# Kernel tuning notes

Hardware: AMD Instinct MI355X
Metric: run time of the kernel (lower is better)

## Reference

```python
import math
import jax, jax.numpy as jnp
import numpy as np
from jax.scipy.special import erf

D = 128                # cubic box / image size (even)
B, T = 4, 2            # particles, candidate poses per particle
GRID_DIST_DEGS = 8.0
GRID_STEP_DEGS = 2.0
PIXEL_SIZE = 1.5       # Angstrom / px
MAX_SHIFT_FRACTION = 0.2
TOP_K = 2
HALF_PARTICLE = 0.5 * D


def _rot_z(a):
    c, s = jnp.cos(a), jnp.sin(a)
    z, o = jnp.zeros_like(a), jnp.ones_like(a)
    return jnp.stack([jnp.stack([c, -s, z], -1),
                      jnp.stack([s, c, z], -1),
                      jnp.stack([z, z, o], -1)], -2)


def _rot_y(a):
    c, s = jnp.cos(a), jnp.sin(a)
    z, o = jnp.zeros_like(a), jnp.ones_like(a)
    return jnp.stack([jnp.stack([c, z, s], -1),
                      jnp.stack([z, o, z], -1),
                      jnp.stack([-s, z, c], -1)], -2)


def _euler_zyz_to_matrix(ang):
    # RELION convention ZYZ: R = Rz(a) @ Ry(b) @ Rz(c)
    return _rot_z(ang[..., 0]) @ _rot_y(ang[..., 1]) @ _rot_z(ang[..., 2])


def _so3_grid_rotmats():
    n = math.ceil(GRID_DIST_DEGS / GRID_STEP_DEGS)
    n = n if n % 2 == 1 else n + 1
    half = GRID_DIST_DEGS / 2.0
    a = np.linspace(-half, half, n)
    g = np.stack(np.meshgrid(a, a, a, indexing='ij'), -1).reshape(-1, 3)
    return _euler_zyz_to_matrix(jnp.deg2rad(jnp.asarray(g, jnp.float32)))


def _compute_dft(vol):
    # sinc^2 gridding pre-filter, then fftshifted rfftn of fftshifted volume
    d = vol.shape[-1]
    f = jnp.fft.fftshift(jnp.fft.fftfreq(d)).astype(vol.dtype)
    fz, fy, fx = jnp.meshgrid(f, f, f, indexing='ij')
    r = jnp.sqrt(fz * fz + fy * fy + fx * fx)
    vol = vol * jnp.sinc(r) ** 2
    dft = jnp.fft.rfftn(jnp.fft.fftshift(vol, axes=(-3, -2, -1)), axes=(-3, -2, -1))
    return jnp.fft.fftshift(dft, axes=(-3, -2))


def _trilinear_complex(vol, z, y, x):
    # trilinear interpolation into a complex 3D array, zero outside bounds
    Dz, Dy, Dx = vol.shape
    z0f, y0f, x0f = jnp.floor(z), jnp.floor(y), jnp.floor(x)
    fz, fy, fx = z - z0f, y - y0f, x - x0f
    z0, y0, x0 = z0f.astype(jnp.int32), y0f.astype(jnp.int32), x0f.astype(jnp.int32)

    def corner(zi, yi, xi, w):
        valid = (zi >= 0) & (zi < Dz) & (yi >= 0) & (yi < Dy) & (xi >= 0) & (xi < Dx)
        v = vol[jnp.clip(zi, 0, Dz - 1), jnp.clip(yi, 0, Dy - 1), jnp.clip(xi, 0, Dx - 1)]
        return jnp.where(valid, v * w, jnp.zeros((), vol.dtype))

    out = corner(z0, y0, x0, (1 - fz) * (1 - fy) * (1 - fx))
    out = out + corner(z0, y0, x0 + 1, (1 - fz) * (1 - fy) * fx)
    out = out + corner(z0, y0 + 1, x0, (1 - fz) * fy * (1 - fx))
    out = out + corner(z0, y0 + 1, x0 + 1, (1 - fz) * fy * fx)
    out = out + corner(z0 + 1, y0, x0, fz * (1 - fy) * (1 - fx))
    out = out + corner(z0 + 1, y0, x0 + 1, fz * (1 - fy) * fx)
    out = out + corner(z0 + 1, y0 + 1, x0, fz * fy * (1 - fx))
    out = out + corner(z0 + 1, y0 + 1, x0 + 1, fz * fy * fx)
    return out


def _extract_central_slices_rfft_3d(vol_rfft, d, rotmats):
    # rotated central-slice extraction from a fftshifted rfft 3D volume
    fy = jnp.fft.fftshift(jnp.fft.fftfreq(d)).astype(jnp.float32)
    fx = jnp.fft.rfftfreq(d).astype(jnp.float32)
    gy, gx = jnp.meshgrid(fy, fx, indexing='ij')            # (H, Wr)
    coords = jnp.stack([jnp.zeros_like(gy), gy, gx], -1)    # zyx, z=0 plane
    Rzyx = rotmats[..., ::-1, ::-1]                         # xyz rotmat -> zyx
    rot = jnp.einsum('...ij,hwj->...hwi', Rzyx, coords)     # (...,H,Wr,3)
    conj_mask = rot[..., 2] < 0                             # redundant half
    rot = jnp.where(conj_mask[..., None], -rot, rot)
    zi = rot[..., 0] * d + d // 2
    yi = rot[..., 1] * d + d // 2
    xi = rot[..., 2] * d
    s = _trilinear_complex(vol_rfft, zi, yi, xi)
    return jnp.where(conj_mask, jnp.conj(s), s)


def _forward(vol, imgs, ctf, rotmats, grid_rotmats):
    d = vol.shape[-1]
    vol_rfft = _compute_dft(vol)                            # (d, d, d//2+1)
    # _real_to_fourier
    fimg = jnp.fft.fftshift(
        jnp.fft.rfftn(jnp.fft.fftshift(imgs, axes=(-2, -1)), axes=(-2, -1)),
        axes=(-2,))                                         # (B, d, d//2+1)
    # compose pose candidates with the local SO3 grid: rotmats @ grid_rotmats
    exp_R = jnp.einsum('gjk,btij->btgik', grid_rotmats, rotmats)   # (B,T,G,3,3)
    projs = _extract_central_slices_rfft_3d(vol_rfft, d, exp_R)    # (B,T,G,H,Wr)
    projs = projs * ctf[:, None, None]
    # correlate_dft_2d
    prod = fimg[:, None, None] * jnp.conj(projs)
    prod = jnp.fft.ifftshift(prod, axes=(-2,))
    corrs = jnp.fft.ifftshift(jnp.fft.irfftn(prod, s=(d, d), axes=(-2, -1)),
                              axes=(-2, -1))                # (B,T,G,d,d) real
    # constrained peak search within max_shift_fraction window
    delta = math.ceil(d * (1.0 - MAX_SHIFT_FRACTION) / 2)
    h0 = delta
    c = corrs[..., h0:d - delta, h0:d - delta]
    maxJ = jnp.max(c, -1)
    argJ = jnp.argmax(c, -1)
    perImgCorr = jnp.max(maxJ, -1)                          # (B,T,G)
    argI = jnp.argmax(maxJ, -1)
    col = jnp.take_along_axis(argJ, argI[..., None], -1)[..., 0]
    shiftsXY = jnp.stack([h0 + col, h0 + argI], -1)         # (B,T,G,2) as (x,y)
    b = perImgCorr.shape[0]
    nrots = perImgCorr.shape[2]
    flat = perImgCorr.reshape(b, -1)                        # (B, T*G)
    maxCorrs, maxIdxs = jax.lax.top_k(flat, TOP_K)
    bestShifts = jnp.take_along_axis(shiftsXY.reshape(b, -1, 2),
                                     maxIdxs[..., None], axis=1)   # (B,K,2)
    mean = jnp.mean(flat, -1, keepdims=True)
    std = jnp.std(flat, -1, keepdims=True, ddof=1)
    comparedWeight = 0.5 * (1.0 + erf((maxCorrs - mean) / (std * 1.4142135623730951)))
    predShiftsAngs = -(bestShifts.astype(jnp.float32) - HALF_PARTICLE) * PIXEL_SIZE
    predRotMats = grid_rotmats[maxIdxs % nrots]             # (B,K,3,3)
    return maxCorrs, predRotMats, predShiftsAngs, comparedWeight


def setup_inputs() -> dict:
    key = jax.random.key(0)
    kv, ki, kc, kr = jax.random.split(key, 4)
    vol = jax.random.normal(kv, (D, D, D), jnp.float32)
    imgs = jax.random.normal(ki, (B, D, D), jnp.float32)
    ctf = jax.random.uniform(kc, (B, D, D // 2 + 1), jnp.float32, -1.0, 1.0)
    ang = jax.random.uniform(kr, (B, T, 3), jnp.float32, -np.pi, np.pi)
    rotmats = _euler_zyz_to_matrix(ang)
    grid_rotmats = _so3_grid_rotmats()
    return {"vol": vol, "imgs": imgs, "ctf": ctf, "rotmats": rotmats,
            "grid_rotmats": grid_rotmats}


def reference(vol, imgs, ctf, rotmats, grid_rotmats):
    return _forward(vol, imgs, ctf, rotmats, grid_rotmats)
```

## Files before the change

kernel.cpp:

```cpp
#include <hip/hip_runtime.h>
#include <math.h>
#include <float.h>

#define DD   128
#define KX   65
#define NB   4
#define NTT  2
#define NG   125
#define NBTG (NB*NTT*NG)
#define WIN  24
#define H0   52

#define PZ  132
#define PY  132
#define PX  68
#define PROW  PX
#define PPLANE (PY*PX)

typedef float f4 __attribute__((ext_vector_type(4), aligned(8)));

__device__ __forceinline__ float2 cmul(float2 a, float2 b){
    return make_float2(a.x*b.x - a.y*b.y, a.x*b.y + a.y*b.x);
}

__device__ __forceinline__ void make_tw(float2* sTw, int tid){
    if (tid < 128){
        float s, c;
        sincosf((float)tid * (float)(M_PI/64.0), &s, &c);
        sTw[tid] = make_float2(c, s);
    }
}

__global__ __launch_bounds__(256) void k_stageA(const float* __restrict__ vol,
                       const float* __restrict__ imgs,
                       float2* __restrict__ A1, float2* __restrict__ B1){
    __shared__ float2 sZ [16*DD];
    __shared__ float2 sZ2[16*DD];
    __shared__ float2 sTw[128];
    int tid = threadIdx.x;
    int bid = blockIdx.x;
    make_tw(sTw, tid);
    __syncthreads();

    if (bid < 512){
        int z = bid >> 2, q = bid & 3;
        int y0 = q*32;
        float fz = (z-64)*(1.0f/128.0f);
        for (int i = tid; i < 16*DD; i += 256){
            int p = i >> 7, x = i & 127;
            int yA = y0 + 2*p;
            float fx = (x-64)*(1.0f/128.0f);
            float fyA = (yA-64)*(1.0f/128.0f);
            float fyB = fyA + (1.0f/128.0f);
            float b2 = fz*fz + fx*fx;
            float rA = sqrtf(b2 + fyA*fyA);
            float rB = sqrtf(b2 + fyB*fyB);
            float sA = (rA > 0.f) ? (sinf((float)M_PI*rA)/((float)M_PI*rA)) : 1.f;
            float sB = (rB > 0.f) ? (sinf((float)M_PI*rB)/((float)M_PI*rB)) : 1.f;
            float a = vol[(z*DD + yA)*DD + x] * sA * sA;
            float b = vol[(z*DD + yA+1)*DD + x] * sB * sB;
            sZ[i] = make_float2(a, b);
        }
        __syncthreads();
        for (int i = tid; i < 16*32; i += 256){
            int p = i >> 5, x1 = i & 31;
            int b0 = p*DD + x1;
            float2 a = sZ[b0], bb = sZ[b0+32], c2 = sZ[b0+64], d = sZ[b0+96];
            float acx=a.x+c2.x, acy=a.y+c2.y;
            float amx=a.x-c2.x, amy=a.y-c2.y;
            float bdx=bb.x+d.x, bdy=bb.y+d.y;
            float bmx=bb.x-d.x, bmy=bb.y-d.y;
            sZ[b0   ] = make_float2(acx+bdx, acy+bdy);
            sZ[b0+32] = make_float2(amx+bmy, amy-bmx);
            sZ[b0+64] = make_float2(acx-bdx, acy-bdy);
            sZ[b0+96] = make_float2(amx-bmy, amy+bmx);
        }
        __syncthreads();
        for (int i = tid; i < 16*32; i += 256){
            int p = i >> 5, r5 = i & 31;
            int c = r5 >> 3, x2 = r5 & 7;
            int b0 = p*DD + 32*c + x2;
            float2 u0 = sZ[b0], u1 = sZ[b0+8], u2 = sZ[b0+16], u3 = sZ[b0+24];
            float2 w1 = sTw[(8*c)&127];  w1.y = -w1.y;
            float2 w2 = sTw[(16*c)&127]; w2.y = -w2.y;
            float2 w3 = sTw[(24*c)&127]; w3.y = -w3.y;
            float2 t1 = cmul(u1,w1), t2 = cmul(u2,w2), t3 = cmul(u3,w3);
            float2 pp = make_float2(u0.x+t2.x, u0.y+t2.y);
            float2 qq = make_float2(u0.x-t2.x, u0.y-t2.y);
            float2 rr = make_float2(t1.x+t3.x, t1.y+t3.y);
            float2 ss = make_float2(t1.x-t3.x, t1.y-t3.y);
            sZ[b0   ] = make_float2(pp.x+rr.x, pp.y+rr.y);
            sZ[b0+8 ] = make_float2(qq.x+ss.y, qq.y-ss.x);
            sZ[b0+16] = make_float2(pp.x-rr.x, pp.y-rr.y);
            sZ[b0+24] = make_float2(qq.x-ss.y, qq.y+ss.x);
        }
        __syncthreads();
        for (int i = tid; i < 16*DD; i += 256){
            int p = i >> 7, k = i & 127;
            int c = k & 3, s = (k >> 2) & 3;
            const float2* v = &sZ[p*DD + 32*c + 8*s];
            float ar0=0,ai0=0,ar1=0,ai1=0;
            int j = 0;
            #pragma unroll
            for (int x2 = 0; x2 < 8; x2 += 2){
                float2 v0 = v[x2], v1 = v[x2+1];
                float2 e0 = sTw[j]; int jn = (j + k)&127;
                float2 e1 = sTw[jn];
                ar0 += v0.x*e0.x + v0.y*e0.y;  ai0 += v0.y*e0.x - v0.x*e0.y;
                ar1 += v1.x*e1.x + v1.y*e1.y;  ai1 += v1.y*e1.x - v1.x*e1.y;
                j = (jn + k)&127;
            }
            sZ2[i] = make_float2(ar0+ar1, ai0+ai1);
        }
        __syncthreads();
        for (int i = tid; i < 16*KX; i += 256){
            int p = i / KX, k = i - p*KX;
            float2 Zk = sZ2[p*DD + k];
            float2 Zm = sZ2[p*DD + ((128-k)&127)];
            float2 A = make_float2(0.5f*(Zk.x+Zm.x), 0.5f*(Zk.y-Zm.y));
            float Dx = Zk.x - Zm.x, Dy = Zk.y + Zm.y;
            float2 Bv = make_float2(0.5f*Dy, -0.5f*Dx);
            int yA = y0 + 2*p;
            A1[(z*DD + yA  )*KX + k] = A;
            A1[(z*DD + yA+1)*KX + k] = Bv;
        }
    } else {
        int o = (bid - 512)*256 + tid;
        if (o >= NB*DD*KX) return;
        int b = o / (DD*KX);
        int r = o - b*DD*KX;
        int y = r / KX, k = r - y*KX;
        const float* row = imgs + (b*DD + y)*DD;
        float ar0=0,ai0=0,ar1=0,ai1=0,ar2=0,ai2=0,ar3=0,ai3=0;
        int i0=0, i1=k&127, i2=(2*k)&127, i3=(3*k)&127;
        int st = (4*k)&127;
        for (int x = 0; x < DD; x += 4){
            float v0=row[x], v1=row[x+1], v2=row[x+2], v3=row[x+3];
            float2 e0=sTw[i0], e1=sTw[i1], e2=sTw[i2], e3=sTw[i3];
            ar0 += v0*e0.x; ai0 -= v0*e0.y;
            ar1 += v1*e1.x; ai1 -= v1*e1.y;
            ar2 += v2*e2.x; ai2 -= v2*e2.y;
            ar3 += v3*e3.x; ai3 -= v3*e3.y;
            i0=(i0+st)&127; i1=(i1+st)&127; i2=(i2+st)&127; i3=(i3+st)&127;
        }
        B1[o] = make_float2(ar0+ar1+ar2+ar3, ai0+ai1+ai2+ai3);
    }
}

__global__ __launch_bounds__(256) void k_stageB(const float2* __restrict__ A1,
                       const float* __restrict__ ctf, const float2* __restrict__ B1,
                       float2* __restrict__ A2, float2* __restrict__ Fc){
    __shared__ float2 sU[32*KX];
    __shared__ float2 sTw[128];
    int tid = threadIdx.x;
    int bid = blockIdx.x;
    make_tw(sTw, tid);
    __syncthreads();

    if (bid < 512){
        int z = bid >> 2, c = bid & 3;
        const float2* base = A1 + z*DD*KX;
        for (int i = tid; i < 32*KX; i += 256){
            int n = i / KX, kk = i - n*KX;
            float2 a  = base[(n    )*KX + kk];
            float2 bb = base[(n+32)*KX + kk];
            float2 c2 = base[(n+64)*KX + kk];
            float2 d  = base[(n+96)*KX + kk];
            float acx = a.x + c2.x, acy = a.y + c2.y;
            float amx = a.x - c2.x, amy = a.y - c2.y;
            float bdx = bb.x + d.x, bdy = bb.y + d.y;
            float bmx = bb.x - d.x, bmy = bb.y - d.y;
            float2 u;
            if (c == 0)      u = make_float2(acx + bdx, acy + bdy);
            else if (c == 2) u = make_float2(acx - bdx, acy - bdy);
            else if (c == 1) u = make_float2(amx + bmy, amy - bmx);
            else             u = make_float2(amx - bmy, amy + bmx);
            sU[i] = u;
        }
        __syncthreads();
        float2 w1 = sTw[(8*c)&127];  w1.y = -w1.y;
        float2 w2 = sTw[(16*c)&127]; w2.y = -w2.y;
        float2 w3 = sTw[(24*c)&127]; w3.y = -w3.y;
        for (int i = tid; i < 8*KX; i += 256){
            int n2 = i / KX, kk = i - n2*KX;
            int b0 = n2*KX + kk;
            float2 u0 = sU[b0], u1 = sU[b0+8*KX], u2 = sU[b0+16*KX], u3 = sU[b0+24*KX];
            float2 t1 = cmul(u1,w1), t2 = cmul(u2,w2), t3 = cmul(u3,w3);
            float2 p = make_float2(u0.x+t2.x, u0.y+t2.y);
            float2 q = make_float2(u0.x-t2.x, u0.y-t2.y);
            float2 r = make_float2(t1.x+t3.x, t1.y+t3.y);
            float2 s = make_float2(t1.x-t3.x, t1.y-t3.y);
            sU[b0       ] = make_float2(p.x+r.x, p.y+r.y);
            sU[b0+ 8*KX ] = make_float2(q.x+s.y, q.y-s.x);
            sU[b0+16*KX ] = make_float2(p.x-r.x, p.y-r.y);
            sU[b0+24*KX ] = make_float2(q.x-s.y, q.y+s.x);
        }
        __syncthreads();
        for (int o = tid; o < 32*KX; o += 256){
            int m = o / KX, kk = o - m*KX;
            int ky = 4*m + c;
            int s4 = m & 3;
            const float2* v = &sU[(8*s4)*KX + kk];
            float ar0=0,ai0=0,ar1=0,ai1=0;
            int j = 0;
            #pragma unroll
            for (int n2 = 0; n2 < 8; n2 += 2){
                float2 v0 = v[n2*KX], v1 = v[(n2+1)*KX];
                float2 e0 = sTw[j]; int jn = (j + ky)&127;
                float2 e1 = sTw[jn];
                ar0 += v0.x*e0.x + v0.y*e0.y;  ai0 += v0.y*e0.x - v0.x*e0.y;
                ar1 += v1.x*e1.x + v1.y*e1.y;  ai1 += v1.y*e1.x - v1.x*e1.y;
                j = (jn + ky)&127;
            }
            A2[(z*DD + ky)*KX + kk] = make_float2(ar0+ar1, ai0+ai1);
        }
    } else {
        int o = (bid - 512)*256 + tid;
        if (o >= NB*DD*KX) return;
        int b = o / (DD*KX);
        int r = o - b*DD*KX;
        int h = r / KX, k = r - h*KX;
        int kky = (h + 64) & 127;
        const float2* col = B1 + b*DD*KX + k;
        float ar0=0,ai0=0,ar1=0,ai1=0,ar2=0,ai2=0,ar3=0,ai3=0;
        int i0=0, i1=kky&127, i2=(2*kky)&127, i3=(3*kky)&127;
        int st = (4*kky)&127;
        for (int y = 0; y < DD; y += 4){
            float2 v0=col[(y+0)*KX], v1=col[(y+1)*KX];
            float2 v2=col[(y+2)*KX], v3=col[(y+3)*KX];
            float2 e0=sTw[i0], e1=sTw[i1], e2=sTw[i2], e3=sTw[i3];
            ar0 += v0.x*e0.x + v0.y*e0.y;  ai0 += v0.y*e0.x - v0.x*e0.y;
            ar1 += v1.x*e1.x + v1.y*e1.y;  ai1 += v1.y*e1.x - v1.x*e1.y;
            ar2 += v2.x*e2.x + v2.y*e2.y;  ai2 += v2.y*e2.x - v2.x*e2.y;
            ar3 += v3.x*e3.x + v3.y*e3.y;  ai3 += v3.y*e3.x - v3.x*e3.y;
            i0=(i0+st)&127; i1=(i1+st)&127; i2=(i2+st)&127; i3=(i3+st)&127;
        }
        float sgn = ((h + k)&1) ? -1.f : 1.f;
        float cf = ctf[o];
        Fc[o] = make_float2((ar0+ar1+ar2+ar3)*sgn*cf, (ai0+ai1+ai2+ai3)*sgn*cf);
    }
}

__global__ __launch_bounds__(256) void k_volD(const float2* __restrict__ A2,
                       float2* __restrict__ VrP){
    __shared__ float2 sU[32*KX];
    __shared__ float2 sTw[128];
    int tid = threadIdx.x;
    int bid = blockIdx.x;
    int ky = bid >> 2, c = bid & 3;
    make_tw(sTw, tid);
    __syncthreads();
    const float2* base = A2 + ky*KX;
    for (int i = tid; i < 32*KX; i += 256){
        int n = i / KX, kk = i - n*KX;
        float2 a  = base[(n    )*DD*KX + kk];
        float2 bb = base[(n+32)*DD*KX + kk];
        float2 c2 = base[(n+64)*DD*KX + kk];
        float2 d  = base[(n+96)*DD*KX + kk];
        float acx = a.x + c2.x, acy = a.y + c2.y;
        float amx = a.x - c2.x, amy = a.y - c2.y;
        float bdx = bb.x + d.x, bdy = bb.y + d.y;
        float bmx = bb.x - d.x, bmy = bb.y - d.y;
        float2 u;
        if (c == 0)      u = make_float2(acx + bdx, acy + bdy);
        else if (c == 2) u = make_float2(acx - bdx, acy - bdy);
        else if (c == 1) u = make_float2(amx + bmy, amy - bmx);
        else             u = make_float2(amx - bmy, amy + bmx);
        sU[i] = u;
    }
    __syncthreads();
    float2 w1 = sTw[(8*c)&127];  w1.y = -w1.y;
    float2 w2 = sTw[(16*c)&127]; w2.y = -w2.y;
    float2 w3 = sTw[(24*c)&127]; w3.y = -w3.y;
    for (int i = tid; i < 8*KX; i += 256){
        int n2 = i / KX, kk = i - n2*KX;
        int b0 = n2*KX + kk;
        float2 u0 = sU[b0], u1 = sU[b0+8*KX], u2 = sU[b0+16*KX], u3 = sU[b0+24*KX];
        float2 t1 = cmul(u1,w1), t2 = cmul(u2,w2), t3 = cmul(u3,w3);
        float2 p = make_float2(u0.x+t2.x, u0.y+t2.y);
        float2 q = make_float2(u0.x-t2.x, u0.y-t2.y);
        float2 r = make_float2(t1.x+t3.x, t1.y+t3.y);
        float2 s = make_float2(t1.x-t3.x, t1.y-t3.y);
        sU[b0       ] = make_float2(p.x+r.x, p.y+r.y);
        sU[b0+ 8*KX ] = make_float2(q.x+s.y, q.y-s.x);
        sU[b0+16*KX ] = make_float2(p.x-r.x, p.y-r.y);
        sU[b0+24*KX ] = make_float2(q.x-s.y, q.y+s.x);
    }
    __syncthreads();
    int hy = (ky + 64) & 127;
    for (int o = tid; o < 32*KX; o += 256){
        int m = o / KX, kk = o - m*KX;
        int kz = 4*m + c;
        int hz = (kz + 64) & 127;
        int s4 = m & 3;
        const float2* v = &sU[(8*s4)*KX + kk];
        float ar0=0,ai0=0,ar1=0,ai1=0;
        int j = 0;
        #pragma unroll
        for (int n2 = 0; n2 < 8; n2 += 2){
            float2 v0 = v[n2*KX], v1 = v[(n2+1)*KX];
            float2 e0 = sTw[j]; int jn = (j + kz)&127;
            float2 e1 = sTw[jn];
            ar0 += v0.x*e0.x + v0.y*e0.y;  ai0 += v0.y*e0.x - v0.x*e0.y;
            ar1 += v1.x*e1.x + v1.y*e1.y;  ai1 += v1.y*e1.x - v1.x*e1.y;
            j = (jn + kz)&127;
        }
        float sgn = ((hz + hy + kk) & 1) ? -1.f : 1.f;
        VrP[((hz+1)*PY + (hy+1))*PX + kk] = make_float2((ar0+ar1)*sgn, (ai0+ai1)*sgn);
    }
}

__global__ __launch_bounds__(256,4) void k_main(
    const float2* __restrict__ VrP, const float2* __restrict__ Fc,
    const float* __restrict__ rotm, const float* __restrict__ grid,
    float* __restrict__ resVal, int2* __restrict__ resShift)
{
    __shared__ float2 sP[DD*17];
    __shared__ float2 sT[WIN*KX];
    __shared__ float2 sTw[128];
    __shared__ float  sM[9];
    __shared__ float  swv[4];
    __shared__ int    swi[4];

    int tid = threadIdx.x;
    int blk = blockIdx.x;
    int b  = blk / (NTT*NG);
    int rr = blk - b*NTT*NG;
    int t  = rr / NG;
    int g  = rr - t*NG;

    make_tw(sTw, tid);
    if (tid < 9){
        int i = tid/3, k = tid - 3*i;
        const float* R  = rotm + (b*NTT + t)*9;
        const float* Gm = grid + g*9;
        sM[tid] = R[i*3+0]*Gm[0*3+k] + R[i*3+1]*Gm[1*3+k] + R[i*3+2]*Gm[2*3+k];
    }
    __syncthreads();

    float M00=sM[0], M01=sM[1], M10=sM[3], M11=sM[4], M20=sM[6], M21=sM[7];
    const float2* FcB = Fc + b*DD*KX;

    const int KB[4]  = {0,17,34,51};
    const int NKc[4] = {17,17,17,14};
    #pragma unroll
    for (int cc = 0; cc < 4; ++cc){
        const int kbase = KB[cc];
        const int Nk    = NKc[cc];

        #pragma unroll 2
        for (int idx = tid; idx < DD*Nk; idx += 256){
            int h = idx / Nk, kk = idx - h*Nk;
            int w = kbase + kk;
            float hf = (float)(h - 64);
            float wf = (float)w;
            float xi = M01*hf + M00*wf;
            float zi = M21*hf + M20*wf + 64.f;
            float yi = M11*hf + M10*wf + 64.f;
            bool neg = xi < 0.f;
            if (neg){ xi = -xi; zi = 128.f - zi; yi = 128.f - yi; }
            xi = fminf(xi, 65.f);
            zi = fminf(fmaxf(zi, -1.f), 129.f);
            yi = fminf(fmaxf(yi, -1.f), 129.f);
            float z0f = floorf(zi), y0f = floorf(yi), x0f = floorf(xi);
            float fz2 = zi - z0f, fy2 = yi - y0f, fx2 = xi - x0f;
            int z0 = (int)z0f, y0 = (int)y0f, x0 = (int)x0f;
            int basei = ((z0+1)*PY + (y0+1))*PX + x0;
            f4 v00 = *reinterpret_cast<const f4*>(VrP + basei);
            f4 v01 = *reinterpret_cast<const f4*>(VrP + basei + PROW);
            f4 v10 = *reinterpret_cast<const f4*>(VrP + basei + PPLANE);
            f4 v11 = *reinterpret_cast<const f4*>(VrP + basei + PPLANE + PROW);
            float2 f = FcB[h*KX + w];
            float gx = 1.f - fx2;
            float r00 = v00.x*gx + v00.z*fx2, i00 = v00.y*gx + v00.w*fx2;
            float r01 = v01.x*gx + v01.z*fx2, i01 = v01.y*gx + v01.w*fx2;
            float r10 = v10.x*gx + v10.z*fx2, i10 = v10.y*gx + v10.w*fx2;
            float r11 = v11.x*gx + v11.z*fx2, i11 = v11.y*gx + v11.w*fx2;
            float gz = 1.f - fz2, gy = 1.f - fy2;
            float w00 = gz*gy, w01 = gz*fy2, w10 = fz2*gy, w11 = fz2*fy2;
            float sr = r00*w00 + r01*w01 + r10*w10 + r11*w11;
            float si = i00*w00 + i01*w01 + i10*w10 + i11*w11;
            if (neg) si = -si;
            sP[h*17 + kk] = make_float2(f.x*sr + f.y*si, f.y*sr - f.x*si);
        }
        __syncthreads();

        for (int i = tid; i < 32*Nk; i += 256){
            int n = i / Nk, kk = i - n*Nk;
            int o0 = n*17 + kk;
            float2 a  = sP[o0];
            float2 bb = sP[o0 + 32*17];
            float2 c2 = sP[o0 + 64*17];
            float2 d  = sP[o0 + 96*17];
            float acx = a.x + c2.x, acy = a.y + c2.y;
            float amx = a.x - c2.x, amy = a.y - c2.y;
            float bdx = bb.x + d.x, bdy = bb.y + d.y;
            float bmx = bb.x - d.x, bmy = bb.y - d.y;
            sP[o0        ] = make_float2(acx + bdx, acy + bdy);
            sP[o0 + 32*17] = make_float2(amx - bmy, amy + bmx);
            sP[o0 + 64*17] = make_float2(acx - bdx, acy - bdy);
            sP[o0 + 96*17] = make_float2(amx + bmy, amy - bmx);
        }
        __syncthreads();

        for (int i = tid; i < 32*Nk; i += 256){
            int q = i / Nk, kk = i - q*Nk;
            int c = q >> 3, n2 = q & 7;
            int b0 = (32*c + n2)*17 + kk;
            float2 u0 = sP[b0], u1 = sP[b0+8*17], u2 = sP[b0+16*17], u3 = sP[b0+24*17];
            float2 w1 = sTw[(8*c)&127], w2 = sTw[(16*c)&127], w3 = sTw[(24*c)&127];
            float2 t1 = cmul(u1,w1), t2 = cmul(u2,w2), t3 = cmul(u3,w3);
            float2 p  = make_float2(u0.x+t2.x, u0.y+t2.y);
            float2 qq = make_float2(u0.x-t2.x, u0.y-t2.y);
            float2 r  = make_float2(t1.x+t3.x, t1.y+t3.y);
            float2 s  = make_float2(t1.x-t3.x, t1.y-t3.y);
            sP[b0       ] = make_float2(p.x+r.x,  p.y+r.y);
            sP[b0+ 8*17 ] = make_float2(qq.x-s.y, qq.y+s.x);
            sP[b0+16*17 ] = make_float2(p.x-r.x,  p.y-r.y);
            sP[b0+24*17 ] = make_float2(qq.x+s.y, qq.y-s.x);
        }
        __syncthreads();

        for (int o = tid; o < WIN*Nk; o += 256){
            int a = o / Nk, kk = o - a*Nk;
            int ry = (116 + a) & 127;
            int c = ry & 3, s4 = (ry >> 2) & 3;
            const float2* v = &sP[(32*c + 8*s4)*17 + kk];
            float ar0=0,ai0=0,ar1=0,ai1=0;
            int j = 0;
            #pragma unroll
            for (int n2 = 0; n2 < 8; n2 += 2){
                float2 v0 = v[n2*17], v1 = v[(n2+1)*17];
                float2 e0 = sTw[j]; int jn = (j + ry)&127;
                float2 e1 = sTw[jn];
                ar0 += v0.x*e0.x - v0.y*e0.y;  ai0 += v0.x*e0.y + v0.y*e0.x;
                ar1 += v1.x*e1.x - v1.y*e1.y;  ai1 += v1.x*e1.y + v1.y*e1.x;
                j = (jn + ry)&127;
            }
            float sgn = (a & 1) ? -(1.f/128.f) : (1.f/128.f);
            sT[a*KX + kbase + kk] = make_float2((ar0+ar1)*sgn, (ai0+ai1)*sgn);
        }
        __syncthreads();
    }

    float2* sPf = sP;
    for (int o = tid; o < WIN*31; o += 256){
        int a = o / 31, km1 = o - a*31;
        int k = km1 + 1;
        const float2* Trow = &sT[a*KX];
        float2 T1 = Trow[k], T2 = Trow[64-k];
        sPf[a*31 + km1]       = make_float2(T1.x + T2.x, T1.y - T2.y);
        sPf[744 + a*31 + km1] = make_float2(T1.x - T2.x, T1.y + T2.y);
    }
    __syncthreads();

    float* sC = reinterpret_cast<float*>(sP + 1488);
    for (int o = tid; o < WIN*WIN; o += 256){
        int a = o / WIN, bx = o - a*WIN;
        int rx = (116 + bx) & 127;
        const float2* Trow = &sT[a*KX];
        float2 T32 = Trow[32];
        float base = Trow[0].x + ((bx & 1) ? -Trow[64].x : Trow[64].x);
        int r4 = rx & 3;
        base += (r4==0) ?  2.f*T32.x : (r4==1) ? -2.f*T32.y
              : (r4==2) ? -2.f*T32.x :  2.f*T32.y;
        const float2* A = sPf + ((bx & 1) ? 744 : 0) + a*31 - 1;
        float acc0=0.f, acc1=0.f;
        int j1 = rx, j2 = (2*rx)&127;
        int st = (2*rx)&127;
        for (int k = 1; k < 31; k += 2){
            float2 e1 = sTw[j1]; float2 A1v = A[k];
            float2 e2 = sTw[j2]; float2 A2v = A[k+1];
            acc0 += A1v.x*e1.x - A1v.y*e1.y;
            acc1 += A2v.x*e2.x - A2v.y*e2.y;
            j1=(j1+st)&127; j2=(j2+st)&127;
        }
        {
            float2 e = sTw[(31*rx)&127]; float2 Av = A[31];
            acc0 += Av.x*e.x - Av.y*e.y;
        }
        sC[o] = (base + 2.f*(acc0+acc1))*(1.f/128.f);
    }
    __syncthreads();

    float best = -FLT_MAX; int bidx = 0x7fffffff;
    for (int i = tid; i < WIN*WIN; i += 256){
        float v = sC[i];
        if (v > best){ best = v; bidx = i; }
    }
    #pragma unroll
    for (int s = 32; s > 0; s >>= 1){
        float ov = __shfl_xor(best, s, 64);
        int   oi = __shfl_xor(bidx, s, 64);
        if (ov > best || (ov == best && oi < bidx)){ best = ov; bidx = oi; }
    }
    if ((tid & 63) == 0){ swv[tid>>6] = best; swi[tid>>6] = bidx; }
    __syncthreads();
    if (tid == 0){
        float bv = swv[0]; int bi = swi[0];
        #pragma unroll
        for (int w2 = 1; w2 < 4; ++w2){
            if (swv[w2] > bv || (swv[w2] == bv && swi[w2] < bi)){ bv = swv[w2]; bi = swi[w2]; }
        }
        int a = bi / WIN, bx = bi - a*WIN;
        resVal[blk] = bv;
        resShift[blk] = make_int2(H0 + bx, H0 + a);
    }
}

__global__ __launch_bounds__(256) void k_final(const float* __restrict__ resVal,
                        const int2* __restrict__ resShift,
                        const float* __restrict__ grid, float* __restrict__ out)
{
    __shared__ float sv[256];
    __shared__ int   si[256];
    __shared__ float sr[256];
    __shared__ float sMean;
    const int N = NTT*NG;
    int b = blockIdx.x, tid = threadIdx.x;
    const float* v = resVal + b*N;
    float myv = (tid < N) ? v[tid] : -FLT_MAX;

    sv[tid] = myv; si[tid] = (tid < N) ? tid : 0x7fffffff;
    __syncthreads();
    for (int s = 128; s > 0; s >>= 1){
        if (tid < s){
            float v2 = sv[tid+s]; int i2 = si[tid+s];
            if (v2 > sv[tid] || (v2 == sv[tid] && i2 < si[tid])){ sv[tid]=v2; si[tid]=i2; }
        }
        __syncthreads();
    }
    float v0 = sv[0]; int i0 = si[0];
    __syncthreads();

    bool act = (tid < N) && (tid != i0);
    sv[tid] = act ? myv : -FLT_MAX; si[tid] = act ? tid : 0x7fffffff;
    __syncthreads();
    for (int s = 128; s > 0; s >>= 1){
        if (tid < s){
            float v2 = sv[tid+s]; int i2 = si[tid+s];
            if (v2 > sv[tid] || (v2 == sv[tid] && i2 < si[tid])){ sv[tid]=v2; si[tid]=i2; }
        }
        __syncthreads();
    }
    float v1 = sv[0]; int i1 = si[0];
    __syncthreads();

    sr[tid] = (tid < N) ? myv : 0.f;
    __syncthreads();
    for (int s = 128; s > 0; s >>= 1){
        if (tid < s) sr[tid] += sr[tid+s];
        __syncthreads();
    }
    if (tid == 0) sMean = sr[0] / (float)N;
    __syncthreads();
    float mean = sMean;

    float d = (tid < N) ? (myv - mean) : 0.f;
    sr[tid] = d*d;
    __syncthreads();
    for (int s = 128; s > 0; s >>= 1){
        if (tid < s) sr[tid] += sr[tid+s];
        __syncthreads();
    }

    if (tid == 0){
        float stdv = sqrtf(sr[0] / (float)(N - 1));
        float vals[2] = {v0, v1};
        int   idxs[2] = {i0, i1};
        for (int k = 0; k < 2; ++k){
            out[b*2 + k] = vals[k];
            int gi = idxs[k] % NG;
            for (int j = 0; j < 9; ++j) out[8 + (b*2+k)*9 + j] = grid[gi*9 + j];
            int2 sh = resShift[b*N + idxs[k]];
            out[80 + (b*2+k)*2 + 0] = -((float)sh.x - 64.f)*1.5f;
            out[80 + (b*2+k)*2 + 1] = -((float)sh.y - 64.f)*1.5f;
            out[96 + b*2 + k] = 0.5f*(1.f + erff((vals[k] - mean)/(stdv*1.41421356237309515f)));
        }
    }
}

extern "C" void kernel_launch(void* const* d_in, const int* in_sizes, int n_in,
                              void* d_out, int out_size, void* d_ws, size_t ws_size,
                              hipStream_t stream)
{
    const float* vol  = (const float*)d_in[0];
    const float* imgs = (const float*)d_in[1];
    const float* ctf  = (const float*)d_in[2];
    const float* rotm = (const float*)d_in[3];
    const float* grid = (const float*)d_in[4];
    float* out = (float*)d_out;

    const size_t A1_BYTES  = (size_t)DD*DD*KX*sizeof(float2);
    const size_t B1_BYTES  = (size_t)NB*DD*KX*sizeof(float2);
    const size_t VRP_BYTES = (size_t)PZ*PY*PX*sizeof(float2);

    char* ws = (char*)d_ws;
    float2* A1  = (float2*)(ws);
    float2* B1  = (float2*)(ws + A1_BYTES);
    float2* VrP = (float2*)(ws);
    size_t off = VRP_BYTES;
    float2* A2 = (float2*)(ws + off); off += A1_BYTES;
    float2* Fc = (float2*)(ws + off); off += B1_BYTES;
    float* resVal = (float*)(ws + off); off += (size_t)NBTG*sizeof(float);
    int2* resShift = (int2*)(ws + off); off += (size_t)NBTG*sizeof(int2);

    k_stageA<<<642, 256, 0, stream>>>(vol, imgs, A1, B1);
    k_stageB<<<642, 256, 0, stream>>>(A1, ctf, B1, A2, Fc);
    hipMemsetAsync(VrP, 0, VRP_BYTES, stream);
    k_volD  <<<512, 256, 0, stream>>>(A2, VrP);
    k_main  <<<NBTG,256, 0, stream>>>(VrP, Fc, rotm, grid, resVal, resShift);
    k_final <<<NB,  256, 0, stream>>>(resVal, resShift, grid, out);
}
```

Baseline: 121.1 us.

## Zero only VrP halo in volD, remap main block order, batch gather loads

Drops the full-volume memset of the padded volume and has k_volD zero only the halo cells that the interior writes never touch. k_main's block index is permuted so that consecutive blocks come from different particle/pose combinations, which changes cache locality across workgroups. The gather loop is manually unrolled so each thread issues two points' worth of trilinear loads before doing any arithmetic, exposing more memory-level parallelism. The risks are higher register pressure and correctness depending on the halo index math exactly covering all uncovered cells.

Measured after the change: 119.2 us. Within noise of the previous version (-1.6%).

```diff
diff --git a/kernel.cpp b/kernel.cpp
--- a/kernel.cpp
+++ b/kernel.cpp
@@ -16,6 +16,7 @@
 #define PX  68
 #define PROW  PX
 #define PPLANE (PY*PX)
+#define HALO_N 119872
 
 typedef float f4 __attribute__((ext_vector_type(4), aligned(8)));
 
@@ -249,7 +250,39 @@
     int bid = blockIdx.x;
     int ky = bid >> 2, c = bid & 3;
     make_tw(sTw, tid);
-    __syncthreads();
+
+    {
+        int hidx = bid*234 + tid;
+        hidx = bid*256 + tid;
+        if (hidx < HALO_N){
+            int z, y, x;
+            if (hidx < 35904){
+                int p = hidx / 8976;
+                int r = hidx - p*8976;
+                z = (p == 0) ? 0 : (128 + p);
+                y = r / 68;
+                x = r - 68*y;
+            } else if (hidx < 70720){
+                int h2 = hidx - 35904;
+                int zz = h2 / 272;
+                int r = h2 - zz*272;
+                z = 1 + zz;
+                int p = r / 68;
+                y = (p == 0) ? 0 : (128 + p);
+                x = r - 68*p;
+            } else {
+                int h3 = hidx - 70720;
+                int zz = h3 / 384;
+                int r = h3 - zz*384;
+                z = 1 + zz;
+                y = 1 + r/3;
+                x = 65 + (r - 3*(r/3));
+            }
+            VrP[(z*PY + y)*PX + x] = make_float2(0.f, 0.f);
+        }
+    }
+    __syncthreads();
+
     const float2* base = A2 + ky*KX;
     for (int i = tid; i < 32*KX; i += 256){
         int n = i / KX, kk = i - n*KX;
@@ -323,7 +356,8 @@
     __shared__ int    swi[4];
 
     int tid = threadIdx.x;
-    int blk = blockIdx.x;
+    int nb  = blockIdx.x;
+    int blk = (nb & 7)*125 + (nb >> 3);
     int b  = blk / (NTT*NG);
     int rr = blk - b*NTT*NG;
     int t  = rr / NG;
@@ -347,41 +381,82 @@
     for (int cc = 0; cc < 4; ++cc){
         const int kbase = KB[cc];
         const int Nk    = NKc[cc];
-
-        #pragma unroll 2
-        for (int idx = tid; idx < DD*Nk; idx += 256){
-            int h = idx / Nk, kk = idx - h*Nk;
-            int w = kbase + kk;
-            float hf = (float)(h - 64);
-            float wf = (float)w;
-            float xi = M01*hf + M00*wf;
-            float zi = M21*hf + M20*wf + 64.f;
-            float yi = M11*hf + M10*wf + 64.f;
-            bool neg = xi < 0.f;
-            if (neg){ xi = -xi; zi = 128.f - zi; yi = 128.f - yi; }
-            xi = fminf(xi, 65.f);
-            zi = fminf(fmaxf(zi, -1.f), 129.f);
-            yi = fminf(fmaxf(yi, -1.f), 129.f);
-            float z0f = floorf(zi), y0f = floorf(yi), x0f = floorf(xi);
-            float fz2 = zi - z0f, fy2 = yi - y0f, fx2 = xi - x0f;
-            int z0 = (int)z0f, y0 = (int)y0f, x0 = (int)x0f;
-            int basei = ((z0+1)*PY + (y0+1))*PX + x0;
-            f4 v00 = *reinterpret_cast<const f4*>(VrP + basei);
-            f4 v01 = *reinterpret_cast<const f4*>(VrP + basei + PROW);
-            f4 v10 = *reinterpret_cast<const f4*>(VrP + basei + PPLANE);
-            f4 v11 = *reinterpret_cast<const f4*>(VrP + basei + PPLANE + PROW);
-            float2 f = FcB[h*KX + w];
-            float gx = 1.f - fx2;
-            float r00 = v00.x*gx + v00.z*fx2, i00 = v00.y*gx + v00.w*fx2;
-            float r01 = v01.x*gx + v01.z*fx2, i01 = v01.y*gx + v01.w*fx2;
-            float r10 = v10.x*gx + v10.z*fx2, i10 = v10.y*gx + v10.w*fx2;
-            float r11 = v11.x*gx + v11.z*fx2, i11 = v11.y*gx + v11.w*fx2;
-            float gz = 1.f - fz2, gy = 1.f - fy2;
-            float w00 = gz*gy, w01 = gz*fy2, w10 = fz2*gy, w11 = fz2*fy2;
-            float sr = r00*w00 + r01*w01 + r10*w10 + r11*w11;
-            float si = i00*w00 + i01*w01 + i10*w10 + i11*w11;
-            if (neg) si = -si;
-            sP[h*17 + kk] = make_float2(f.x*sr + f.y*si, f.y*sr - f.x*si);
+        const int total = DD*Nk;
+
+        for (int base = 0; base < total; base += 512){
+            int iA = base + tid;
+            int iB = iA + 256;
+            bool vA = iA < total, vB = iB < total;
+            int cA = vA ? iA : 0, cB = vB ? iB : 0;
+
+            int hA = cA / Nk, kkA = cA - hA*Nk;  int wA = kbase + kkA;
+            int hB = cB / Nk, kkB = cB - hB*Nk;  int wB = kbase + kkB;
+
+            float hfA = (float)(hA - 64), wfA = (float)wA;
+            float xiA = M01*hfA + M00*wfA;
+            float ziA = M21*hfA + M20*wfA + 64.f;
+            float yiA = M11*hfA + M10*wfA + 64.f;
+            bool negA = xiA < 0.f;
+            if (negA){ xiA = -xiA; ziA = 128.f - ziA; yiA = 128.f - yiA; }
+            xiA = fminf(xiA, 65.f);
+            ziA = fminf(fmaxf(ziA, -1.f), 129.f);
+            yiA = fminf(fmaxf(yiA, -1.f), 129.f);
+            float zfA = floorf(ziA), yfA = floorf(yiA), xfA = floorf(xiA);
+            float fzA = ziA - zfA, fyA = yiA - yfA, fxA = xiA - xfA;
+            int z0A = (int)zfA, y0A = (int)yfA, x0A = (int)xfA;
+            int baseiA = ((z0A+1)*PY + (y0A+1))*PX + x0A;
+
+            float hfB = (float)(hB - 64), wfB = (float)wB;
+            float xiB = M01*hfB + M00*wfB;
+            float ziB = M21*hfB + M20*wfB + 64.f;
+            float yiB = M11*hfB + M10*wfB + 64.f;
+            bool negB = xiB < 0.f;
+            if (negB){ xiB = -xiB; ziB = 128.f - ziB; yiB = 128.f - yiB; }
+            xiB = fminf(xiB, 65.f);
+            ziB = fminf(fmaxf(ziB, -1.f), 129.f);
+            yiB = fminf(fmaxf(yiB, -1.f), 129.f);
+            float zfB = floorf(ziB), yfB = floorf(yiB), xfB = floorf(xiB);
+            float fzB = ziB - zfB, fyB = yiB - yfB, fxB = xiB - xfB;
+            int z0B = (int)zfB, y0B = (int)yfB, x0B = (int)xfB;
+            int baseiB = ((z0B+1)*PY + (y0B+1))*PX + x0B;
+
+            f4 a00 = *reinterpret_cast<const f4*>(VrP + baseiA);
+            f4 a01 = *reinterpret_cast<const f4*>(VrP + baseiA + PROW);
+            f4 a10 = *reinterpret_cast<const f4*>(VrP + baseiA + PPLANE);
+            f4 a11 = *reinterpret_cast<const f4*>(VrP + baseiA + PPLANE + PROW);
+            f4 b00 = *reinterpret_cast<const f4*>(VrP + baseiB);
+            f4 b01 = *reinterpret_cast<const f4*>(VrP + baseiB + PROW);
+            f4 b10 = *reinterpret_cast<const f4*>(VrP + baseiB + PPLANE);
+            f4 b11 = *reinterpret_cast<const f4*>(VrP + baseiB + PPLANE + PROW);
+            float2 fA = FcB[hA*KX + wA];
+            float2 fB = FcB[hB*KX + wB];
+
+            {
+                float gx = 1.f - fxA;
+                float r00 = a00.x*gx + a00.z*fxA, i00 = a00.y*gx + a00.w*fxA;
+                float r01 = a01.x*gx + a01.z*fxA, i01 = a01.y*gx + a01.w*fxA;
+                float r10 = a10.x*gx + a10.z*fxA, i10 = a10.y*gx + a10.w*fxA;
+                float r11 = a11.x*gx + a11.z*fxA, i11 = a11.y*gx + a11.w*fxA;
+                float gz = 1.f - fzA, gy = 1.f - fyA;
+                float w00 = gz*gy, w01 = gz*fyA, w10 = fzA*gy, w11 = fzA*fyA;
+                float sr = r00*w00 + r01*w01 + r10*w10 + r11*w11;
+                float si = i00*w00 + i01*w01 + i10*w10 + i11*w11;
+                if (negA) si = -si;
+                if (vA) sP[hA*17 + kkA] = make_float2(fA.x*sr + fA.y*si, fA.y*sr - fA.x*si);
+            }
+            {
+                float gx = 1.f - fxB;
+                float r00 = b00.x*gx + b00.z*fxB, i00 = b00.y*gx + b00.w*fxB;
+                float r01 = b01.x*gx + b01.z*fxB, i01 = b01.y*gx + b01.w*fxB;
+                float r10 = b10.x*gx + b10.z*fxB, i10 = b10.y*gx + b10.w*fxB;
+                float r11 = b11.x*gx + b11.z*fxB, i11 = b11.y*gx + b11.w*fxB;
+                float gz = 1.f - fzB, gy = 1.f - fyB;
+                float w00 = gz*gy, w01 = gz*fyB, w10 = fzB*gy, w11 = fzB*fyB;
+                float sr = r00*w00 + r01*w01 + r10*w10 + r11*w11;
+                float si = i00*w00 + i01*w01 + i10*w10 + i11*w11;
+                if (negB) si = -si;
+                if (vB) sP[hB*17 + kkB] = make_float2(fB.x*sr + fB.y*si, fB.y*sr - fB.x*si);
+            }
         }
         __syncthreads();
 
@@ -607,7 +682,6 @@
 
     k_stageA<<<642, 256, 0, stream>>>(vol, imgs, A1, B1);
     k_stageB<<<642, 256, 0, stream>>>(A1, ctf, B1, A2, Fc);
-    hipMemsetAsync(VrP, 0, VRP_BYTES, stream);
     k_volD  <<<512, 256, 0, stream>>>(A2, VrP);
     k_main  <<<NBTG,256, 0, stream>>>(VrP, Fc, rotm, grid, resVal, resShift);
     k_final <<<NB,  256, 0, stream>>>(resVal, resShift, grid, out);
```
